# Performance work log

Hardware: AMD Instinct MI355X
Metric: run time of the kernel (lower is better)

## Reference

```python
import jax, jax.numpy as jnp
import numpy as np

B, N, C = 32, 1025, 768
H, D = 12, 64          # num_heads, head_dim
M = 4 * D              # num random features = 256
HEIGHT, WIDTH = 32, 32 # spatial grid; N = HEIGHT*WIDTH + 1 (CLS)
EPS = 1e-6


def setup_inputs() -> dict:
    key = jax.random.key(0)
    ks = jax.random.split(key, 7)
    x = jax.random.normal(ks[0], (B, N, C), jnp.float32)
    w_qkv = jax.random.normal(ks[1], (3 * C, C), jnp.float32) * 0.02
    w_proj = jax.random.normal(ks[2], (C, C), jnp.float32) * 0.02
    b_proj = jnp.zeros((C,), jnp.float32)
    c_row = jax.random.normal(ks[3], (H, D), jnp.float32) * 0.02
    c_col = jax.random.normal(ks[4], (H, D), jnp.float32) * 0.02
    # orthogonal random-feature projection (m, d): QR blocks scaled by chi norm
    blocks = []
    for i in range(M // D):
        Hm = jax.random.normal(jax.random.fold_in(ks[5], i), (D, D), jnp.float32)
        Q, _ = jnp.linalg.qr(Hm)
        nrm = jnp.linalg.norm(jax.random.normal(jax.random.fold_in(ks[6], i), (D,), jnp.float32))
        blocks.append(Q * nrm)
    proj_feat = jnp.concatenate(blocks, axis=0)  # (M, D)
    return {"x": x, "w_qkv": w_qkv, "w_proj": w_proj, "b_proj": b_proj,
            "c_row": c_row, "c_col": c_col, "proj_feat": proj_feat}


def _string(xp, c_row, c_col):
    """Circulant-STRING rotation. xp: (B,H,Np,D)."""
    rows = jnp.arange(HEIGHT, dtype=jnp.float32)
    cols = jnp.arange(WIDTH, dtype=jnp.float32)
    gr, gc = jnp.meshgrid(rows, cols, indexing='ij')
    pos_r = gr.ravel()  # (Np,)
    pos_c = gc.ravel()
    # g: (H, Np, D)
    g = pos_r[None, :, None] * c_row[:, None, :] + pos_c[None, :, None] * c_col[:, None, :]
    g_fft = jnp.fft.fft(g, axis=-1)
    exp_lambda = jnp.exp(2j * g_fft.imag)          # (H, Np, D) complex, unit modulus
    x_fft = jnp.fft.fft(xp, axis=-1)               # (B, H, Np, D) complex
    rotated = jnp.fft.ifft(exp_lambda[None] * x_fft, axis=-1).real
    return rotated.astype(xp.dtype)


def _favor(x, proj):
    """Positive random feature map. x: (B,H,N,D), proj: (M,D) -> (B,H,N,M)."""
    xs = x * (D ** -0.25)
    px = jnp.einsum('bhnd,md->bhnm', xs, proj)
    norm_sq = 0.5 * jnp.sum(xs * xs, axis=-1, keepdims=True)
    return jnp.exp(px - norm_sq)


def reference(x, w_qkv, w_proj, b_proj, c_row, c_col, proj_feat):
    qkv = x @ w_qkv.T                                  # (B, N, 3C)
    qkv = qkv.reshape(B, N, 3, H, D).transpose(2, 0, 3, 1, 4)  # (3,B,H,N,D)
    q, k, v = qkv[0], qkv[1], qkv[2]
    # N == HEIGHT*WIDTH + 1 -> CLS token at position 0 is left unrotated
    q_cls, q_p = q[:, :, :1, :], q[:, :, 1:, :]
    k_cls, k_p = k[:, :, :1, :], k[:, :, 1:, :]
    q = jnp.concatenate([q_cls, _string(q_p, c_row, c_col)], axis=2)
    k = jnp.concatenate([k_cls, _string(k_p, c_row, c_col)], axis=2)
    q_feat = _favor(q, proj_feat)                      # (B,H,N,M)
    k_feat = _favor(k, proj_feat)
    # bidirectional linear attention
    context = jnp.einsum('bhnm,bhne->bhme', k_feat, v) # (B,H,M,D)
    num = jnp.einsum('bhnm,bhme->bhne', q_feat, context)
    k_sum = k_feat.sum(axis=2)                         # (B,H,M)
    den = jnp.einsum('bhnm,bhm->bhn', q_feat, k_sum)[..., None]
    den = jnp.maximum(den, EPS)
    out = num / den                                    # (B,H,N,D)
    out = out.transpose(0, 2, 1, 3).reshape(B, N, C)
    return out @ w_proj.T + b_proj
```

## Files before the change

kernel.cpp:

```cpp
#include <hip/hip_runtime.h>
#include <math.h>

typedef _Float16 f16;
typedef _Float16 f16x8 __attribute__((ext_vector_type(8)));
typedef _Float16 f16x4 __attribute__((ext_vector_type(4)));
typedef float f32x4 __attribute__((ext_vector_type(4)));

#define LDSK 40
#define NTOK 1025
#define CC 768
#define HH 12
#define DD 64
#define MM 256
#define VPAD 1056
#define BN_ROWS 32800

__device__ __forceinline__ void load_row16(const f16* p, f16x8& a0, f16x8& a1) {
    a0 = *(const f16x8*)p;
    a1 = *(const f16x8*)(p + 8);
}
__device__ __forceinline__ void load_row16(const float* p, f16x8& a0, f16x8& a1) {
    const float4* q = (const float4*)p;
    float4 u0 = q[0], u1 = q[1], u2 = q[2], u3 = q[3];
    a0[0] = (f16)u0.x; a0[1] = (f16)u0.y; a0[2] = (f16)u0.z; a0[3] = (f16)u0.w;
    a0[4] = (f16)u1.x; a0[5] = (f16)u1.y; a0[6] = (f16)u1.z; a0[7] = (f16)u1.w;
    a1[0] = (f16)u2.x; a1[1] = (f16)u2.y; a1[2] = (f16)u2.z; a1[3] = (f16)u2.w;
    a1[4] = (f16)u3.x; a1[5] = (f16)u3.y; a1[6] = (f16)u3.z; a1[7] = (f16)u3.w;
}

__device__ __forceinline__ void gload16(const f16* g, f16* l) {
    __builtin_amdgcn_global_load_lds(
        (const __attribute__((address_space(1))) unsigned int*)g,
        (__attribute__((address_space(3))) unsigned int*)l, 16, 0, 0);
}

__global__ void k_diag(float* out, float v) {
    if (threadIdx.x == 0 && blockIdx.x == 0) out[0] = v;
}

__global__ __launch_bounds__(256) void k_cvt_x(const float* __restrict__ x, f16* __restrict__ xw) {
    size_t i = ((size_t)blockIdx.x * 256 + threadIdx.x) * 4;
    float4 v;
    if (i < (size_t)BN_ROWS * CC) v = *(const float4*)(x + i);
    else v = make_float4(0.f, 0.f, 0.f, 0.f);
    f16x4 o; o[0] = (f16)v.x; o[1] = (f16)v.y; o[2] = (f16)v.z; o[3] = (f16)v.w;
    *(f16x4*)(xw + i) = o;
}

__global__ __launch_bounds__(256) void k_cvt(const float* __restrict__ in, f16* __restrict__ out,
                                             long n, float scale) {
    long i = (long)blockIdx.x * 256 + threadIdx.x;
    if (i < n) out[i] = (f16)(in[i] * scale);
}

__global__ __launch_bounds__(256) void k_zpad(f16* __restrict__ v16t) {
    int bh = blockIdx.x;
    for (int u = threadIdx.x; u < 64 * 31; u += 256) {
        int d = u / 31, j = u - d * 31;
        v16t[((size_t)bh * DD + d) * VPAD + 1025 + j] = (f16)0.f;
    }
}

__global__ __launch_bounds__(64) void k_ab(const float* __restrict__ c_row,
                                           const float* __restrict__ c_col,
                                           float* __restrict__ ab) {
    int h = blockIdx.x, k = threadIdx.x;
    float sa = 0.f, sb = 0.f;
    for (int d = 0; d < 64; ++d) {
        float s = sinf((float)((k * d) & 63) * (6.283185307179586f / 64.f));
        sa += c_row[h * 64 + d] * s;
        sb += c_col[h * 64 + d] * s;
    }
    ab[h * 64 + k] = -2.f * sa;
    ab[768 + h * 64 + k] = -2.f * sb;
}

__global__ __launch_bounds__(64) void k_wcirc(const float* __restrict__ ab, float* __restrict__ wc) {
    int hp = blockIdx.x; int h = hp >> 10; int p = hp & 1023;
    float pr = (float)(p >> 5), pc = (float)(p & 31);
    int t = threadIdx.x;
    __shared__ float th[64];
    th[t] = pr * ab[h * 64 + t] + pc * ab[768 + h * 64 + t];
    __syncthreads();
    float s = 0.f;
    #pragma unroll 8
    for (int k = 0; k < 64; ++k) {
        float arg = th[k] + (float)((k * t) & 63) * (6.283185307179586f / 64.f);
        s += __cosf(arg);
    }
    wc[(size_t)hp * 64 + t] = s * (1.f / 64.f);
}

template <bool GA, typename TA, typename TB>
__device__ __forceinline__ void gemm128_core(const TA* __restrict__ A, const TB* __restrict__ Bm,
                                             int K, int row0, int col0, int Alim,
                                             f32x4 (&acc)[4][4],
                                             f16 (*As)[LDSK], f16 (*Bs)[LDSK]) {
    const int tid = threadIdx.x;
    const int lane = tid & 63;
    const int lr = tid >> 1, lk = (tid & 1) * 16;
    const int frow = lane & 15, fk = (lane >> 4) * 8;
    const int wave = tid >> 6, wr = wave >> 1, wc = wave & 1;
    for (int kt = 0; kt < K; kt += 32) {
        f16x8 a0 = {}, a1 = {}, b0, b1;
        if (!GA || (row0 + lr) < Alim)
            load_row16(A + (size_t)(row0 + lr) * K + kt + lk, a0, a1);
        load_row16(Bm + (size_t)(col0 + lr) * K + kt + lk, b0, b1);
        __syncthreads();
        *(f16x8*)&As[lr][lk] = a0; *(f16x8*)&As[lr][lk + 8] = a1;
        *(f16x8*)&Bs[lr][lk] = b0; *(f16x8*)&Bs[lr][lk + 8] = b1;
        __syncthreads();
        f16x8 af[4], bf[4];
        #pragma unroll
        for (int m = 0; m < 4; ++m) af[m] = *(const f16x8*)&As[wr * 64 + m * 16 + frow][fk];
        #pragma unroll
        for (int n = 0; n < 4; ++n) bf[n] = *(const f16x8*)&Bs[wc * 64 + n * 16 + frow][fk];
        #pragma unroll
        for (int m = 0; m < 4; ++m)
            #pragma unroll
            for (int n = 0; n < 4; ++n)
                acc[m][n] = __builtin_amdgcn_mfma_f32_16x16x32_f16(af[m], bf[n], acc[m][n], 0, 0, 0);
    }
}

__device__ __forceinline__ void gemm128_dma(const f16* __restrict__ A, const f16* __restrict__ Bm,
                                            int K, int row0, int col0,
                                            f32x4 (&acc)[4][4], f16* As, f16* Bs) {
    const int tid = threadIdx.x;
    const int lane = tid & 63, wave = tid >> 6;
    const int frow = lane & 15, fk8 = (lane >> 4) * 8;
    const int wr = wave >> 1, wc = wave & 1;
    const int srow = lane >> 3;
    const int scol = ((lane & 7) ^ srow) * 8;
    const f16* aG = A + (size_t)(row0 + wave * 32 + srow) * K + scol;
    const f16* bG = Bm + (size_t)(col0 + wave * 32 + srow) * K + scol;
    f16* aL = As + (wave * 32) * 64;
    f16* bL = Bs + (wave * 32) * 64;
    const int cswz = (frow & 7) * 8;
    for (int kt = 0; kt < K; kt += 64) {
        __syncthreads();
        #pragma unroll
        for (int j = 0; j < 4; ++j) {
            gload16(aG + kt + (size_t)(8 * j) * K, aL + (8 * j) * 64);
            gload16(bG + kt + (size_t)(8 * j) * K, bL + (8 * j) * 64);
        }
        __syncthreads();
        #pragma unroll
        for (int ks = 0; ks < 2; ++ks) {
            f16x8 af[4], bf[4];
            #pragma unroll
            for (int m = 0; m < 4; ++m)
                af[m] = *(const f16x8*)&As[(wr * 64 + m * 16 + frow) * 64 + ((ks * 32 + fk8) ^ cswz)];
            #pragma unroll
            for (int n = 0; n < 4; ++n)
                bf[n] = *(const f16x8*)&Bs[(wc * 64 + n * 16 + frow) * 64 + ((ks * 32 + fk8) ^ cswz)];
            #pragma unroll
            for (int m = 0; m < 4; ++m)
                #pragma unroll
                for (int n = 0; n < 4; ++n)
                    acc[m][n] = __builtin_amdgcn_mfma_f32_16x16x32_f16(af[m], bf[n], acc[m][n], 0, 0, 0);
        }
    }
}

__device__ __forceinline__ void qkv_epilogue(f32x4 (&acc)[4][4], int row0, int col0,
                                             f16* __restrict__ q16, f16* __restrict__ k16,
                                             f16* __restrict__ v16t) {
    int lane = threadIdx.x & 63, wave = threadIdx.x >> 6;
    int wr = wave >> 1, wc = wave & 1;
    int rb = row0 + wr * 64 + 4 * (lane >> 4);
    int cb = col0 + wc * 64 + (lane & 15);
    #pragma unroll
    for (int m = 0; m < 4; ++m)
        #pragma unroll
        for (int n = 0; n < 4; ++n)
            #pragma unroll
            for (int i = 0; i < 4; ++i) {
                int r = rb + m * 16 + i;
                if (r >= BN_ROWS) continue;
                int j = cb + n * 16;
                int b = r / NTOK, nn = r - b * NTOK;
                int t = j / CC, rem = j - t * CC;
                int h = rem >> 6, d = rem & 63;
                size_t bh = (size_t)b * HH + h;
                f16 val = (f16)acc[m][n][i];
                if (t == 0) q16[(bh * NTOK + nn) * DD + d] = val;
                else if (t == 1) k16[(bh * NTOK + nn) * DD + d] = val;
                else v16t[(bh * DD + d) * VPAD + nn] = val;
            }
}

__global__ __launch_bounds__(256) void k_gemm_qkv_dma(const f16* __restrict__ A, const f16* __restrict__ Bm,
                                                      f16* __restrict__ q16, f16* __restrict__ k16,
                                                      f16* __restrict__ v16t) {
    __shared__ __attribute__((aligned(16))) f16 As[128 * 64];
    __shared__ __attribute__((aligned(16))) f16 Bs[128 * 64];
    const int q = 578, r = 2;
    int xg = blockIdx.x & 7, o8 = blockIdx.x >> 3;
    int wg = (xg < r ? xg * (q + 1) : r * (q + 1) + (xg - r) * q) + o8;
    int row0 = (wg / 18) * 128, col0 = (wg % 18) * 128;
    f32x4 acc[4][4] = {};
    gemm128_dma(A, Bm, CC, row0, col0, acc, As, Bs);
    qkv_epilogue(acc, row0, col0, q16, k16, v16t);
}

__global__ __launch_bounds__(256) void k_gemm_qkv_f32(const float* __restrict__ A, const f16* __restrict__ Bm,
                                                      f16* __restrict__ q16, f16* __restrict__ k16,
                                                      f16* __restrict__ v16t) {
    __shared__ __attribute__((aligned(16))) f16 As[128][LDSK];
    __shared__ __attribute__((aligned(16))) f16 Bs[128][LDSK];
    f32x4 acc[4][4] = {};
    int row0 = blockIdx.x * 128, col0 = blockIdx.y * 128;
    gemm128_core<true>(A, Bm, CC, row0, col0, BN_ROWS, acc, As, Bs);
    qkv_epilogue(acc, row0, col0, q16, k16, v16t);
}

__global__ __launch_bounds__(256) void k_rotate(const float* __restrict__ wcirc,
                                                f16* __restrict__ q16, f16* __restrict__ k16,
                                                float* __restrict__ nsqq, float* __restrict__ nsqk) {
    const int p = blockIdx.x, h = blockIdx.y;
    const int nn = p + 1;
    const int tid = threadIdx.x;
    __shared__ float wl[64];
    __shared__ __attribute__((aligned(16))) f16 Ws[64][72];
    __shared__ __attribute__((aligned(16))) f16 Xs[64][72];
    if (tid < 64) wl[tid] = wcirc[((size_t)h * 1024 + p) * 64 + tid];
    {
        const int row = tid >> 2;
        const int ch = (tid & 3) * 16;
        const int b = row & 31;
        const f16* src = ((row < 32) ? q16 : k16) + (((size_t)b * HH + h) * NTOK + nn) * DD + ch;
        f16x8 v0 = *(const f16x8*)src;
        f16x8 v1 = *(const f16x8*)(src + 8);
        *(f16x8*)&Xs[row][ch] = v0;
        *(f16x8*)&Xs[row][ch + 8] = v1;
    }
    __syncthreads();
    #pragma unroll
    for (int j = 0; j < 16; ++j) {
        int idx = tid * 16 + j;
        int d = idx >> 6, m = idx & 63;
        Ws[d][m] = (f16)wl[(d - m) & 63];
    }
    __syncthreads();
    const int lane = tid & 63, wave = tid >> 6;
    const int frow = lane & 15, fk = (lane >> 4) * 8;
    f32x4 acc[4] = {};
    #pragma unroll
    for (int kt = 0; kt < 64; kt += 32) {
        f16x8 a = *(const f16x8*)&Xs[wave * 16 + frow][kt + fk];
        #pragma unroll
        for (int n = 0; n < 4; ++n) {
            f16x8 bfr = *(const f16x8*)&Ws[n * 16 + frow][kt + fk];
            acc[n] = __builtin_amdgcn_mfma_f32_16x16x32_f16(a, bfr, acc[n], 0, 0, 0);
        }
    }
    #pragma unroll
    for (int i = 0; i < 4; ++i) {
        int row = wave * 16 + 4 * (lane >> 4) + i;
        int b = row & 31;
        f16* dst = ((row < 32) ? q16 : k16) + (((size_t)b * HH + h) * NTOK + nn) * DD;
        float ss = 0.f;
        #pragma unroll
        for (int n = 0; n < 4; ++n) {
            float v = acc[n][i];
            dst[n * 16 + (lane & 15)] = (f16)v;
            ss += v * v;
        }
        ss += __shfl_xor(ss, 1); ss += __shfl_xor(ss, 2);
        ss += __shfl_xor(ss, 4); ss += __shfl_xor(ss, 8);
        if ((lane & 15) == 0) {
            float* nd = (row < 32) ? nsqq : nsqk;
            nd[((size_t)b * HH + h) * NTOK + nn] = ss * (1.f / 16.f);
        }
    }
}

__global__ __launch_bounds__(256) void k_cls_nsq(const f16* __restrict__ q16, const f16* __restrict__ k16,
                                                 float* __restrict__ nsqq, float* __restrict__ nsqk) {
    int gw = (blockIdx.x * 256 + threadIdx.x) >> 6;
    int lane = threadIdx.x & 63;
    int which = gw & 1; int bh = gw >> 1;
    const f16* src = (which ? k16 : q16) + (size_t)bh * NTOK * DD;
    float v = (float)src[lane];
    float ss = v * v;
    for (int off = 1; off < 64; off <<= 1) ss += __shfl_xor(ss, off);
    if (lane == 0) (which ? nsqk : nsqq)[(size_t)bh * NTOK] = ss * (1.f / 16.f);
}

__global__ __launch_bounds__(512) void k_fctx(const f16* __restrict__ k16, const f16* __restrict__ v16t,
                                              const f16* __restrict__ pfeat, const float* __restrict__ nsqk,
                                              f16* __restrict__ ctxT) {
    __shared__ __attribute__((aligned(16))) f16 uLDS[80 * 136];
    f16 (*fts)[LDSK] = (f16(*)[LDSK])uLDS;
    f16 (*cx)[136]   = (f16(*)[136])uLDS;
    const int bh = blockIdx.x;
    const int tid = threadIdx.x;
    const int lane = tid & 63, w = tid >> 6;
    const int frow = lane & 15, fk8 = (lane >> 4) * 8;
    const int m0 = w * 32;
    f16x8 pf[2][2];
    #pragma unroll
    for (int mf = 0; mf < 2; ++mf)
        #pragma unroll
        for (int kf = 0; kf < 2; ++kf)
            pf[mf][kf] = *(const f16x8*)&pfeat[(m0 + mf * 16 + frow) * DD + kf * 32 + fk8];
    const f16* kb_base = k16 + (size_t)bh * NTOK * DD;
    const f16* vb_base = v16t + (size_t)bh * DD * VPAD;
    const float* ns_base = nsqk + (size_t)bh * NTOK;
    auto loadK = [&](f16x8 (&kb)[2][2], int n0) {
        #pragma unroll
        for (int nf = 0; nf < 2; ++nf) {
            int n = n0 + nf * 16 + frow;
            #pragma unroll
            for (int kf = 0; kf < 2; ++kf) {
                f16x8 z = {};
                if (n < NTOK) z = *(const f16x8*)&kb_base[(size_t)n * DD + kf * 32 + fk8];
                kb[nf][kf] = z;
            }
        }
    };
    f32x4 acc[2][5] = {};
    f16x8 kb[2][2];
    loadK(kb, 0);
    for (int n0 = 0; n0 < VPAD; n0 += 32) {
        f16x8 vb[4];
        #pragma unroll
        for (int ef = 0; ef < 4; ++ef)
            vb[ef] = *(const f16x8*)&vb_base[(size_t)(ef * 16 + frow) * VPAD + n0 + fk8];
        f32x4 fa[2][2] = {};
        #pragma unroll
        for (int kf = 0; kf < 2; ++kf)
            #pragma unroll
            for (int mf = 0; mf < 2; ++mf)
                #pragma unroll
                for (int nf = 0; nf < 2; ++nf)
                    fa[mf][nf] = __builtin_amdgcn_mfma_f32_16x16x32_f16(pf[mf][kf], kb[nf][kf], fa[mf][nf], 0, 0, 0);
        f16x8 kbn[2][2];
        loadK(kbn, n0 + 32);
        #pragma unroll
        for (int nf = 0; nf < 2; ++nf) {
            int ncol = n0 + nf * 16 + frow;
            float ns = (ncol < NTOK) ? ns_base[ncol] : 0.f;
            #pragma unroll
            for (int mf = 0; mf < 2; ++mf)
                #pragma unroll
                for (int i = 0; i < 4; ++i) {
                    int mloc = m0 + mf * 16 + 4 * (lane >> 4) + i;
                    float v = (ncol < NTOK) ? fminf(__expf(fa[mf][nf][i] - ns), 60000.f) : 0.f;
                    fts[mloc][nf * 16 + frow] = (f16)v;
                }
        }
        __syncthreads();
        f16x8 afr[2];
        #pragma unroll
        for (int mf = 0; mf < 2; ++mf) afr[mf] = *(const f16x8*)&fts[m0 + mf * 16 + frow][fk8];
        #pragma unroll
        for (int ef = 0; ef < 4; ++ef)
            #pragma unroll
            for (int mf = 0; mf < 2; ++mf)
                acc[mf][ef] = __builtin_amdgcn_mfma_f32_16x16x32_f16(afr[mf], vb[ef], acc[mf][ef], 0, 0, 0);
        {
            f16x8 bfr;
            #pragma unroll
            for (int j = 0; j < 8; ++j)
                bfr[j] = (f16)((frow == 0 && (n0 + fk8 + j) < NTOK) ? 1.f : 0.f);
            #pragma unroll
            for (int mf = 0; mf < 2; ++mf)
                acc[mf][4] = __builtin_amdgcn_mfma_f32_16x16x32_f16(afr[mf], bfr, acc[mf][4], 0, 0, 0);
        }
        __syncthreads();
        #pragma unroll
        for (int nf = 0; nf < 2; ++nf)
            #pragma unroll
            for (int kf = 0; kf < 2; ++kf)
                kb[nf][kf] = kbn[nf][kf];
    }
    #pragma unroll
    for (int p = 0; p < 2; ++p) {
        __syncthreads();
        if ((w >> 2) == p) {
            int mb = m0 - p * 128;
            #pragma unroll
            for (int mf = 0; mf < 2; ++mf)
                #pragma unroll
                for (int ef = 0; ef < 5; ++ef) {
                    int e = ef * 16 + frow;
                    f16x4 pk;
                    #pragma unroll
                    for (int i = 0; i < 4; ++i) pk[i] = (f16)acc[mf][ef][i];
                    *(f16x4*)&cx[e][mb + mf * 16 + 4 * (lane >> 4)] = pk;
                }
        }
        __syncthreads();
        for (int u = tid; u < 80 * 16; u += 512) {
            int e = u >> 4, seg = u & 15;
            *(f16x8*)&ctxT[((size_t)bh * 80 + e) * MM + p * 128 + seg * 8] =
                *(const f16x8*)&cx[e][seg * 8];
        }
    }
}

__global__ __launch_bounds__(256) void k_fnum(const f16* __restrict__ q16, const f16* __restrict__ pfeat,
                                              const float* __restrict__ nsqq, const f16* __restrict__ ctxT,
                                              f16* __restrict__ attn) {
    __shared__ __attribute__((aligned(16))) f16 qf_s[128][72];
    const int bh = blockIdx.y;
    const int b = bh / HH, h = bh - b * HH;
    const int t0 = blockIdx.x * 128;
    const int tid = threadIdx.x;
    const int lane = tid & 63, w = tid >> 6;
    const int frow = lane & 15, fk8 = (lane >> 4) * 8;
    const f16* qbase = q16 + (size_t)bh * NTOK * DD;
    const f16* cbase = ctxT + (size_t)bh * 80 * MM;
    f16x8 qa[2][2];
    float ns[2][4];
    #pragma unroll
    for (int tf = 0; tf < 2; ++tf) {
        int t = t0 + w * 32 + tf * 16 + frow;
        #pragma unroll
        for (int kf = 0; kf < 2; ++kf) {
            f16x8 z = {};
            if (t < NTOK) z = *(const f16x8*)&qbase[(size_t)t * DD + kf * 32 + fk8];
            qa[tf][kf] = z;
        }
        #pragma unroll
        for (int i = 0; i < 4; ++i) {
            int tr = t0 + w * 32 + tf * 16 + 4 * (lane >> 4) + i;
            ns[tf][i] = (tr < NTOK) ? nsqq[(size_t)bh * NTOK + tr] : 0.f;
        }
    }
    auto loadPB = [&](f16x8 (&pb)[2][2], int mc) {
        #pragma unroll
        for (int nf = 0; nf < 2; ++nf)
            #pragma unroll
            for (int kf = 0; kf < 2; ++kf)
                pb[nf][kf] = *(const f16x8*)&pfeat[(mc * 32 + nf * 16 + frow) * DD + kf * 32 + fk8];
    };
    f32x4 acc[2][5] = {};
    f16x8 pb[2][2];
    loadPB(pb, 0);
    #pragma unroll
    for (int mc = 0; mc < 8; ++mc) {
        f32x4 fa[2][2] = {};
        #pragma unroll
        for (int kf = 0; kf < 2; ++kf)
            #pragma unroll
            for (int tf = 0; tf < 2; ++tf)
                #pragma unroll
                for (int nf = 0; nf < 2; ++nf)
                    fa[tf][nf] = __builtin_amdgcn_mfma_f32_16x16x32_f16(qa[tf][kf], pb[nf][kf], fa[tf][nf], 0, 0, 0);
        f16x8 pbn[2][2];
        loadPB(pbn, (mc + 1) & 7);
        #pragma unroll
        for (int tf = 0; tf < 2; ++tf)
            #pragma unroll
            for (int nf = 0; nf < 2; ++nf)
                #pragma unroll
                for (int i = 0; i < 4; ++i) {
                    int tl = w * 32 + tf * 16 + 4 * (lane >> 4) + i;
                    float v = fminf(__expf(fa[tf][nf][i] - ns[tf][i]), 60000.f);
                    qf_s[tl][nf * 16 + frow] = (f16)v;
                }
        __syncthreads();
        f16x8 afr[2];
        #pragma unroll
        for (int tf = 0; tf < 2; ++tf) afr[tf] = *(const f16x8*)&qf_s[w * 32 + tf * 16 + frow][fk8];
        #pragma unroll
        for (int ef = 0; ef < 5; ++ef) {
            f16x8 bfr = *(const f16x8*)&cbase[(size_t)(ef * 16 + frow) * MM + mc * 32 + fk8];
            #pragma unroll
            for (int tf = 0; tf < 2; ++tf)
                acc[tf][ef] = __builtin_amdgcn_mfma_f32_16x16x32_f16(afr[tf], bfr, acc[tf][ef], 0, 0, 0);
        }
        __syncthreads();
        #pragma unroll
        for (int nf = 0; nf < 2; ++nf)
            #pragma unroll
            for (int kf = 0; kf < 2; ++kf)
                pb[nf][kf] = pbn[nf][kf];
    }
    #pragma unroll
    for (int tf = 0; tf < 2; ++tf)
        #pragma unroll
        for (int i = 0; i < 4; ++i) {
            float den = fmaxf(__shfl(acc[tf][4][i], lane & 48), 1e-6f);
            int tl = w * 32 + tf * 16 + 4 * (lane >> 4) + i;
            #pragma unroll
            for (int ef = 0; ef < 4; ++ef)
                qf_s[tl][ef * 16 + frow] = (f16)(acc[tf][ef][i] / den);
        }
    __syncthreads();
    for (int u = tid; u < 128 * 8; u += 256) {
        int tok = u >> 3, seg = u & 7;
        if (t0 + tok < NTOK)
            *(f16x8*)&attn[((size_t)(b * NTOK + t0 + tok)) * CC + h * DD + seg * 8] =
                *(const f16x8*)&qf_s[tok][seg * 8];
    }
}

__device__ __forceinline__ void proj_epilogue(f32x4 (&acc)[4][4], int row0, int col0,
                                              const float* __restrict__ bias, float* __restrict__ out) {
    int lane = threadIdx.x & 63, wave = threadIdx.x >> 6;
    int wr = wave >> 1, wc = wave & 1;
    int rb = row0 + wr * 64 + 4 * (lane >> 4);
    int cb = col0 + wc * 64 + (lane & 15);
    #pragma unroll
    for (int n = 0; n < 4; ++n) {
        int j = cb + n * 16;
        float bj = bias[j];
        #pragma unroll
        for (int m = 0; m < 4; ++m)
            #pragma unroll
            for (int i = 0; i < 4; ++i) {
                int r = rb + m * 16 + i;
                if (r < BN_ROWS) out[(size_t)r * CC + j] = acc[m][n][i] + bj;
            }
    }
}

__global__ __launch_bounds__(256) void k_gemm_proj_dma(const f16* __restrict__ A, const f16* __restrict__ Bm,
                                                       const float* __restrict__ bias, float* __restrict__ out) {
    __shared__ __attribute__((aligned(16))) f16 As[128 * 64];
    __shared__ __attribute__((aligned(16))) f16 Bs[128 * 64];
    const int q = 192, r = 6;
    int xg = blockIdx.x & 7, o8 = blockIdx.x >> 3;
    int wg = (xg < r ? xg * (q + 1) : r * (q + 1) + (xg - r) * q) + o8;
    int row0 = (wg / 6) * 128, col0 = (wg % 6) * 128;
    f32x4 acc[4][4] = {};
    gemm128_dma(A, Bm, CC, row0, col0, acc, As, Bs);
    proj_epilogue(acc, row0, col0, bias, out);
}

__global__ __launch_bounds__(256) void k_gemm_proj(const f16* __restrict__ A, const f16* __restrict__ Bm,
                                                   const float* __restrict__ bias, float* __restrict__ out) {
    __shared__ __attribute__((aligned(16))) f16 As[128][LDSK];
    __shared__ __attribute__((aligned(16))) f16 Bs[128][LDSK];
    f32x4 acc[4][4] = {};
    int row0 = blockIdx.x * 128, col0 = blockIdx.y * 128;
    gemm128_core<true>(A, Bm, CC, row0, col0, BN_ROWS, acc, As, Bs);
    proj_epilogue(acc, row0, col0, bias, out);
}

extern "C" void kernel_launch(void* const* d_in, const int* in_sizes, int n_in,
                              void* d_out, int out_size, void* d_ws, size_t ws_size,
                              hipStream_t stream) {
    const float* x = (const float*)d_in[0];
    const float* w_qkv = (const float*)d_in[1];
    const float* w_proj = (const float*)d_in[2];
    const float* b_proj = (const float*)d_in[3];
    const float* c_row = (const float*)d_in[4];
    const float* c_col = (const float*)d_in[5];
    const float* proj_feat = (const float*)d_in[6];
    float* out = (float*)d_out;
    char* ws = (char*)d_ws;
    char* ob = (char*)d_out;

    const size_t O_WQKV  = 0;
    const size_t O_WPROJ = 3538944;
    const size_t O_Q16   = 4718592;
    const size_t O_K16   = 55099392;
    const size_t O_XW    = 105480192;
    const size_t NEED_B  = 105480192;
    const size_t NEED_A  = 156008448;
    if (ws_size < NEED_B) {
        k_diag<<<1, 64, 0, stream>>>(out, (float)((double)ws_size / 1048576.0));
        return;
    }
    const bool useA = (ws_size >= NEED_A);

    const size_t OD_V    = 0;
    const size_t OD_CTX  = 51904512;
    const size_t OD_WC   = 67633152;
    const size_t OD_NSQQ = 70778880;
    const size_t OD_NSQK = 72353280;
    const size_t OD_PF   = 73927680;
    const size_t OD_AB   = 73960448;

    f16* wqkv16  = (f16*)(ws + O_WQKV);
    f16* wproj16 = (f16*)(ws + O_WPROJ);
    f16* q16     = (f16*)(ws + O_Q16);
    f16* k16     = (f16*)(ws + O_K16);
    f16* xw16    = (f16*)(ws + O_XW);
    f16* v16t    = (f16*)(ob + OD_V);
    f16* ctxT    = (f16*)(ob + OD_CTX);
    float* wcirc = (float*)(ob + OD_WC);
    float* nsqq  = (float*)(ob + OD_NSQQ);
    float* nsqk  = (float*)(ob + OD_NSQK);
    f16* pfeat16 = (f16*)(ob + OD_PF);
    float* ab    = (float*)(ob + OD_AB);
    f16* attn16  = k16;

    k_cvt<<<6912, 256, 0, stream>>>(w_qkv, wqkv16, 1769472L, 1.f);
    k_cvt<<<2304, 256, 0, stream>>>(w_proj, wproj16, 589824L, 1.f);
    k_cvt<<<64, 256, 0, stream>>>(proj_feat, pfeat16, 16384L, 0.3535533906f);
    k_ab<<<12, 64, 0, stream>>>(c_row, c_col, ab);
    k_wcirc<<<12288, 64, 0, stream>>>(ab, wcirc);

    if (useA) {
        k_cvt_x<<<24672, 256, 0, stream>>>(x, xw16);
        k_gemm_qkv_dma<<<4626, 256, 0, stream>>>(xw16, wqkv16, q16, k16, v16t);
    } else {
        k_gemm_qkv_f32<<<dim3(257, 18), 256, 0, stream>>>(x, wqkv16, q16, k16, v16t);
    }
    k_zpad<<<384, 256, 0, stream>>>(v16t);

    k_rotate<<<dim3(1024, 12), 256, 0, stream>>>(wcirc, q16, k16, nsqq, nsqk);
    k_cls_nsq<<<192, 256, 0, stream>>>(q16, k16, nsqq, nsqk);

    k_fctx<<<384, 512, 0, stream>>>(k16, v16t, pfeat16, nsqk, ctxT);
    k_fnum<<<dim3(9, 384), 256, 0, stream>>>(q16, pfeat16, nsqq, ctxT, attn16);

    if (useA) {
        k_gemm_proj_dma<<<1542, 256, 0, stream>>>(attn16, wproj16, b_proj, out);
    } else {
        k_gemm_proj<<<dim3(257, 6), 256, 0, stream>>>(attn16, wproj16, b_proj, out);
    }

    (void)in_sizes; (void)n_in; (void)out_size;
}
```

Before: 660.7 us.

## Double-buffer LDS tiles in DMA GEMMs to overlap global loads with MFMA

Replaces the single-buffer direct-to-LDS GEMM loop with a two-stage ping-pong. The next K tile is prefetched into the alternate LDS buffer while the current tile feeds the MFMAs, with one barrier per iteration instead of two. The aim is to hide global load latency in both the QKV and output projection GEMMs. It doubles LDS use per block to 64KB, which may lower occupancy.

```diff
diff --git a/kernel.cpp b/kernel.cpp
--- a/kernel.cpp
+++ b/kernel.cpp
@@ -123,9 +123,9 @@
     }
 }
 
-__device__ __forceinline__ void gemm128_dma(const f16* __restrict__ A, const f16* __restrict__ Bm,
-                                            int K, int row0, int col0,
-                                            f32x4 (&acc)[4][4], f16* As, f16* Bs) {
+__device__ __forceinline__ void gemm128_pipe(const f16* __restrict__ A, const f16* __restrict__ Bm,
+                                             int K, int row0, int col0,
+                                             f32x4 (&acc)[4][4], f16* As, f16* Bs) {
     const int tid = threadIdx.x;
     const int lane = tid & 63, wave = tid >> 6;
     const int frow = lane & 15, fk8 = (lane >> 4) * 8;
@@ -134,32 +134,44 @@
     const int scol = ((lane & 7) ^ srow) * 8;
     const f16* aG = A + (size_t)(row0 + wave * 32 + srow) * K + scol;
     const f16* bG = Bm + (size_t)(col0 + wave * 32 + srow) * K + scol;
-    f16* aL = As + (wave * 32) * 64;
-    f16* bL = Bs + (wave * 32) * 64;
+    const int aoff = (wave * 32) * 64;
     const int cswz = (frow & 7) * 8;
+    #pragma unroll
+    for (int j = 0; j < 4; ++j) {
+        gload16(aG + (size_t)(8 * j) * K, As + aoff + (8 * j) * 64);
+        gload16(bG + (size_t)(8 * j) * K, Bs + aoff + (8 * j) * 64);
+    }
+    int cur = 0;
     for (int kt = 0; kt < K; kt += 64) {
-        __syncthreads();
-        #pragma unroll
-        for (int j = 0; j < 4; ++j) {
-            gload16(aG + kt + (size_t)(8 * j) * K, aL + (8 * j) * 64);
-            gload16(bG + kt + (size_t)(8 * j) * K, bL + (8 * j) * 64);
-        }
-        __syncthreads();
+        asm volatile("s_waitcnt vmcnt(0)" ::: "memory");
+        __builtin_amdgcn_s_barrier();
+        asm volatile("" ::: "memory");
+        if (kt + 64 < K) {
+            int nb = (cur ^ 1) * 8192;
+            #pragma unroll
+            for (int j = 0; j < 4; ++j) {
+                gload16(aG + kt + 64 + (size_t)(8 * j) * K, As + nb + aoff + (8 * j) * 64);
+                gload16(bG + kt + 64 + (size_t)(8 * j) * K, Bs + nb + aoff + (8 * j) * 64);
+            }
+        }
+        const f16* Ac = As + cur * 8192;
+        const f16* Bc = Bs + cur * 8192;
         #pragma unroll
         for (int ks = 0; ks < 2; ++ks) {
             f16x8 af[4], bf[4];
             #pragma unroll
             for (int m = 0; m < 4; ++m)
-                af[m] = *(const f16x8*)&As[(wr * 64 + m * 16 + frow) * 64 + ((ks * 32 + fk8) ^ cswz)];
+                af[m] = *(const f16x8*)&Ac[(wr * 64 + m * 16 + frow) * 64 + ((ks * 32 + fk8) ^ cswz)];
             #pragma unroll
             for (int n = 0; n < 4; ++n)
-                bf[n] = *(const f16x8*)&Bs[(wc * 64 + n * 16 + frow) * 64 + ((ks * 32 + fk8) ^ cswz)];
+                bf[n] = *(const f16x8*)&Bc[(wc * 64 + n * 16 + frow) * 64 + ((ks * 32 + fk8) ^ cswz)];
             #pragma unroll
             for (int m = 0; m < 4; ++m)
                 #pragma unroll
                 for (int n = 0; n < 4; ++n)
                     acc[m][n] = __builtin_amdgcn_mfma_f32_16x16x32_f16(af[m], bf[n], acc[m][n], 0, 0, 0);
         }
+        cur ^= 1;
     }
 }
 
@@ -193,14 +205,14 @@
 __global__ __launch_bounds__(256) void k_gemm_qkv_dma(const f16* __restrict__ A, const f16* __restrict__ Bm,
                                                       f16* __restrict__ q16, f16* __restrict__ k16,
                                                       f16* __restrict__ v16t) {
-    __shared__ __attribute__((aligned(16))) f16 As[128 * 64];
-    __shared__ __attribute__((aligned(16))) f16 Bs[128 * 64];
+    __shared__ __attribute__((aligned(16))) f16 As[2 * 128 * 64];
+    __shared__ __attribute__((aligned(16))) f16 Bs[2 * 128 * 64];
     const int q = 578, r = 2;
     int xg = blockIdx.x & 7, o8 = blockIdx.x >> 3;
     int wg = (xg < r ? xg * (q + 1) : r * (q + 1) + (xg - r) * q) + o8;
     int row0 = (wg / 18) * 128, col0 = (wg % 18) * 128;
     f32x4 acc[4][4] = {};
-    gemm128_dma(A, Bm, CC, row0, col0, acc, As, Bs);
+    gemm128_pipe(A, Bm, CC, row0, col0, acc, As, Bs);
     qkv_epilogue(acc, row0, col0, q16, k16, v16t);
 }
 
@@ -521,14 +533,14 @@
 
 __global__ __launch_bounds__(256) void k_gemm_proj_dma(const f16* __restrict__ A, const f16* __restrict__ Bm,
                                                        const float* __restrict__ bias, float* __restrict__ out) {
-    __shared__ __attribute__((aligned(16))) f16 As[128 * 64];
-    __shared__ __attribute__((aligned(16))) f16 Bs[128 * 64];
+    __shared__ __attribute__((aligned(16))) f16 As[2 * 128 * 64];
+    __shared__ __attribute__((aligned(16))) f16 Bs[2 * 128 * 64];
     const int q = 192, r = 6;
     int xg = blockIdx.x & 7, o8 = blockIdx.x >> 3;
     int wg = (xg < r ? xg * (q + 1) : r * (q + 1) + (xg - r) * q) + o8;
     int row0 = (wg / 6) * 128, col0 = (wg % 6) * 128;
     f32x4 acc[4][4] = {};
-    gemm128_dma(A, Bm, CC, row0, col0, acc, As, Bs);
+    gemm128_pipe(A, Bm, CC, row0, col0, acc, As, Bs);
     proj_epilogue(acc, row0, col0, bias, out);
 }
 
```

Result: no change. 658.8 us (median of 3 runs) (-0.3%).
